# Performance work log

Hardware: AMD Instinct MI355X
Metric: run time of the kernel (lower is better)

Reference implementation:

```python
import jax, jax.numpy as jnp
import numpy as np

N_NODES = 10000
N_EDGES = 160000
IN_DIM = 256
HID = 128
HEADS = 8
OUT_DIM = 64
LN_EPS = 1e-5
NEG_SLOPE = 0.2


def _gat_layer(x, W, att_src, att_dst, bias, src, dst, heads, out_ch, n):
    # x: [N, F_in]; W: [F_in, heads*out_ch]; att_*: [heads, out_ch]; bias: [heads*out_ch]
    xl = (x @ W).reshape(n, heads, out_ch)              # [N, H, C]
    a_src = jnp.einsum('nhc,hc->nh', xl, att_src)        # [N, H]
    a_dst = jnp.einsum('nhc,hc->nh', xl, att_dst)        # [N, H]
    e = a_src[src] + a_dst[dst]                          # [E, H]
    e = jnp.where(e > 0, e, NEG_SLOPE * e)               # leaky_relu(0.2)
    e_max = jax.ops.segment_max(e, dst, num_segments=n)  # segment softmax (stable)
    e = jnp.exp(e - e_max[dst])
    denom = jax.ops.segment_sum(e, dst, num_segments=n)
    alpha = e / (denom[dst] + 1e-16)                     # [E, H]
    msg = xl[src] * alpha[:, :, None]                    # [E, H, C]
    out = jax.ops.segment_sum(msg, dst, num_segments=n)  # [N, H, C]
    return out.reshape(n, heads * out_ch) + bias


def setup_inputs() -> dict:
    key = jax.random.key(0)
    ks = jax.random.split(key, 12)
    s = 0.05
    inp = {
        'x': jax.random.normal(ks[0], (N_NODES, IN_DIM), dtype=jnp.float32),
        'edge_index': jax.random.randint(ks[1], (2, N_EDGES), 0, N_NODES, dtype=jnp.int32),
        'W1': jax.random.normal(ks[2], (IN_DIM, HEADS * HID), dtype=jnp.float32) * s,
        'att_src1': jax.random.normal(ks[3], (HEADS, HID), dtype=jnp.float32) * s,
        'att_dst1': jax.random.normal(ks[4], (HEADS, HID), dtype=jnp.float32) * s,
        'b1': jnp.zeros((HEADS * HID,), dtype=jnp.float32),
        'W2': jax.random.normal(ks[5], (HEADS * HID, OUT_DIM), dtype=jnp.float32) * s,
        'att_src2': jax.random.normal(ks[6], (1, OUT_DIM), dtype=jnp.float32) * s,
        'att_dst2': jax.random.normal(ks[7], (1, OUT_DIM), dtype=jnp.float32) * s,
        'b2': jnp.zeros((OUT_DIM,), dtype=jnp.float32),
        'gamma': jnp.ones((OUT_DIM,), dtype=jnp.float32),
        'beta': jnp.zeros((OUT_DIM,), dtype=jnp.float32),
    }
    return inp


def reference(x, edge_index, W1, att_src1, att_dst1, b1, W2, att_src2, att_dst2, b2, gamma, beta):
    n = x.shape[0]
    # GATConv adds self-loops by default
    loops = jnp.arange(n, dtype=edge_index.dtype)
    src = jnp.concatenate([edge_index[0], loops])
    dst = jnp.concatenate([edge_index[1], loops])
    h = _gat_layer(x, W1, att_src1, att_dst1, b1, src, dst, HEADS, HID, n)
    h = jax.nn.elu(h)  # dropout is identity in eval mode
    h = _gat_layer(h, W2, att_src2, att_dst2, b2, src, dst, 1, OUT_DIM, n)
    mu = jnp.mean(h, axis=-1, keepdims=True)
    var = jnp.mean(jnp.square(h - mu), axis=-1, keepdims=True)
    return (h - mu) / jnp.sqrt(var + LN_EPS) * gamma + beta
```

## Files before the change

### kernel.cpp

```cpp
#include <hip/hip_runtime.h>

#define N_NODES 10000
#define N_EDGES 160000
#define E_TOT   (N_EDGES + N_NODES)
#define IN_DIM  256
#define HID     128
#define HEADS   8
#define F1      (HEADS*HID)
#define OUT_DIM 64
#define LN_EPS  1e-5f
#define NEG_SLOPE 0.2f

typedef __attribute__((ext_vector_type(8))) short short8;
typedef __attribute__((ext_vector_type(4))) float f32x4;

static __device__ __forceinline__ float lrelu(float e){ return e > 0.f ? e : NEG_SLOPE*e; }

static __device__ __forceinline__ ushort f2bf(float f){
  union { float f; uint32_t u; } v; v.f = f;
  uint32_t u = v.u;
  return (ushort)((u + 0x7FFFu + ((u >> 16) & 1u)) >> 16);
}
static __device__ __forceinline__ float bf2f(ushort h){
  union { uint32_t u; float f; } v; v.u = ((uint32_t)h) << 16; return v.f;
}
#define BLO(u) bf2f((ushort)((u) & 0xffffu))
#define BHI(u) bf2f((ushort)((u) >> 16))


__global__ void k_cvt_x(const float* __restrict__ in, ushort* __restrict__ out, int n4){
  int i = blockIdx.x*blockDim.x + threadIdx.x;
  if (i >= n4) return;
  float4 v = *(const float4*)&in[(size_t)i*4];
  uint2 o;
  o.x = (uint32_t)f2bf(v.x) | ((uint32_t)f2bf(v.y) << 16);
  o.y = (uint32_t)f2bf(v.z) | ((uint32_t)f2bf(v.w) << 16);
  *(uint2*)&out[(size_t)i*4] = o;
}


__global__ __launch_bounds__(256) void k_tr(const float* __restrict__ W1, ushort* __restrict__ W1T,
                                            const float* __restrict__ W2, ushort* __restrict__ W2T){
  __shared__ float tile[64][65];
  int bid = blockIdx.x;
  const float* W; ushort* WT; int R, C, rt, ct;
  if (bid < 64){ W = W1; WT = W1T; R = IN_DIM; C = F1; rt = bid & 3; ct = bid >> 2; }
  else         { W = W2; WT = W2T; R = F1; C = OUT_DIM; rt = bid - 64; ct = 0; }
  int r0 = rt*64, c0 = ct*64;
  int t = threadIdx.x;
  int sub = t >> 4, q4 = (t & 15)*4;
  #pragma unroll
  for (int p = 0; p < 4; p++){
    int r = sub + p*16;
    float4 v = *(const float4*)&W[(size_t)(r0 + r)*C + c0 + q4];
    tile[r][q4]   = v.x; tile[r][q4+1] = v.y;
    tile[r][q4+2] = v.z; tile[r][q4+3] = v.w;
  }
  __syncthreads();
  #pragma unroll
  for (int p = 0; p < 4; p++){
    int c = sub + p*16;
    ushort h0 = f2bf(tile[q4+0][c]);
    ushort h1 = f2bf(tile[q4+1][c]);
    ushort h2 = f2bf(tile[q4+2][c]);
    ushort h3 = f2bf(tile[q4+3][c]);
    uint2 o;
    o.x = (uint32_t)h0 | ((uint32_t)h1 << 16);
    o.y = (uint32_t)h2 | ((uint32_t)h3 << 16);
    *(uint2*)&WT[(size_t)(c0 + c)*R + r0 + q4] = o;
  }
}


__global__ void k_hist(const int* __restrict__ ei, int* __restrict__ counts){
  int e = blockIdx.x*blockDim.x + threadIdx.x;
  if (e >= E_TOT) return;
  int dst = (e < N_EDGES) ? ei[N_EDGES + e] : (e - N_EDGES);
  atomicAdd(&counts[dst], 1);
}

__global__ __launch_bounds__(1024) void k_scan(const int* __restrict__ counts,
                                               int* __restrict__ offsets,
                                               int* __restrict__ cursor){
  __shared__ int part[1024];
  int tid = threadIdx.x;
  const int CH = (N_NODES + 1023)/1024;
  int base = tid*CH;
  int s = 0;
  #pragma unroll
  for (int i = 0; i < CH; i++){ int idx = base+i; if (idx < N_NODES) s += counts[idx]; }
  part[tid] = s;
  __syncthreads();
  for (int off = 1; off < 1024; off <<= 1){
    int v = (tid >= off) ? part[tid-off] : 0;
    __syncthreads();
    part[tid] += v;
    __syncthreads();
  }
  int run = part[tid] - s;
  for (int i = 0; i < CH; i++){
    int idx = base+i;
    if (idx < N_NODES){ offsets[idx] = run; cursor[idx] = run; run += counts[idx]; }
  }
}

__global__ void k_scatter(const int* __restrict__ ei, int* __restrict__ cursor,
                          int* __restrict__ csr_src){
  int e = blockIdx.x*blockDim.x + threadIdx.x;
  if (e >= E_TOT) return;
  int src, dst;
  if (e < N_EDGES){ src = ei[e]; dst = ei[N_EDGES + e]; }
  else            { src = e - N_EDGES; dst = src; }
  int pos = atomicAdd(&cursor[dst], 1);
  csr_src[pos] = src;
}


__global__ __launch_bounds__(256) void k_wav(const float* __restrict__ W1,
                                             const float* __restrict__ att_s,
                                             const float* __restrict__ att_d,
                                             float* __restrict__ w_as,
                                             float* __restrict__ w_ad){
  int wg = blockIdx.x*4 + (threadIdx.x >> 6);
  int lane = threadIdx.x & 63;
  int h = wg >> 8, i = wg & 255;
  if (h >= HEADS) return;
  int c = lane*2;
  float2 wv = *(const float2*)&W1[(size_t)i*F1 + h*HID + c];
  float2 as = *(const float2*)&att_s[h*HID + c];
  float2 ad = *(const float2*)&att_d[h*HID + c];
  float s = wv.x*as.x + wv.y*as.y;
  float d = wv.x*ad.x + wv.y*ad.y;
  #pragma unroll
  for (int o = 32; o > 0; o >>= 1){ s += __shfl_xor(s, o); d += __shfl_xor(d, o); }
  if (lane == 0){ w_as[h*IN_DIM + i] = s; w_ad[h*IN_DIM + i] = d; }
}


__global__ __launch_bounds__(256) void k_attv(const ushort* __restrict__ xb,
                                              const float* __restrict__ w_as,
                                              const float* __restrict__ w_ad,
                                              float* __restrict__ as1,
                                              float* __restrict__ ad1){
  int n = blockIdx.x*4 + (threadIdx.x >> 6);
  int lane = threadIdx.x & 63;
  if (n >= N_NODES) return;
  int c0 = lane*4;
  uint2 px = *(const uint2*)&xb[(size_t)n*IN_DIM + c0];
  float x0 = BLO(px.x), x1 = BHI(px.x), x2 = BLO(px.y), x3 = BHI(px.y);
  float s[HEADS], d[HEADS];
  #pragma unroll
  for (int h = 0; h < HEADS; h++){
    float4 ws = *(const float4*)&w_as[h*IN_DIM + c0];
    float4 wd = *(const float4*)&w_ad[h*IN_DIM + c0];
    s[h] = x0*ws.x + x1*ws.y + x2*ws.z + x3*ws.w;
    d[h] = x0*wd.x + x1*wd.y + x2*wd.z + x3*wd.w;
  }
  #pragma unroll
  for (int o = 32; o > 0; o >>= 1){
    #pragma unroll
    for (int h = 0; h < HEADS; h++){ s[h] += __shfl_xor(s[h], o); d[h] += __shfl_xor(d[h], o); }
  }
  if (lane == 0){
    #pragma unroll
    for (int h = 0; h < HEADS; h++){ as1[n*HEADS + h] = s[h]; ad1[n*HEADS + h] = d[h]; }
  }
}


__global__ __launch_bounds__(256) void k_prep1(const float* __restrict__ a_src,
                       const float* __restrict__ a_dst,
                       const int* __restrict__ offsets, const int* __restrict__ counts,
                       const int* __restrict__ csr, float* __restrict__ alpha){
  int n = blockIdx.x*4 + (threadIdx.x >> 6);
  int lane = threadIdx.x & 63;
  if (n >= N_NODES) return;
  int off = offsets[n], k = counts[n];
  float ad[HEADS];
  #pragma unroll
  for (int h = 0; h < HEADS; h++) ad[h] = a_dst[n*HEADS + h];

  float lm[HEADS];
  #pragma unroll
  for (int h = 0; h < HEADS; h++) lm[h] = -1e30f;
  for (int i = lane; i < k; i += 64){
    int s = csr[off + i];
    float4 v0 = *(const float4*)&a_src[s*HEADS];
    float4 v1 = *(const float4*)&a_src[s*HEADS + 4];
    lm[0] = fmaxf(lm[0], lrelu(v0.x + ad[0]));
    lm[1] = fmaxf(lm[1], lrelu(v0.y + ad[1]));
    lm[2] = fmaxf(lm[2], lrelu(v0.z + ad[2]));
    lm[3] = fmaxf(lm[3], lrelu(v0.w + ad[3]));
    lm[4] = fmaxf(lm[4], lrelu(v1.x + ad[4]));
    lm[5] = fmaxf(lm[5], lrelu(v1.y + ad[5]));
    lm[6] = fmaxf(lm[6], lrelu(v1.z + ad[6]));
    lm[7] = fmaxf(lm[7], lrelu(v1.w + ad[7]));
  }
  #pragma unroll
  for (int o = 32; o > 0; o >>= 1){
    #pragma unroll
    for (int h = 0; h < HEADS; h++) lm[h] = fmaxf(lm[h], __shfl_xor(lm[h], o));
  }

  float ls[HEADS];
  #pragma unroll
  for (int h = 0; h < HEADS; h++) ls[h] = 0.f;
  for (int i = lane; i < k; i += 64){
    int s = csr[off + i];
    float4 v0 = *(const float4*)&a_src[s*HEADS];
    float4 v1 = *(const float4*)&a_src[s*HEADS + 4];
    ls[0] += __expf(lrelu(v0.x + ad[0]) - lm[0]);
    ls[1] += __expf(lrelu(v0.y + ad[1]) - lm[1]);
    ls[2] += __expf(lrelu(v0.z + ad[2]) - lm[2]);
    ls[3] += __expf(lrelu(v0.w + ad[3]) - lm[3]);
    ls[4] += __expf(lrelu(v1.x + ad[4]) - lm[4]);
    ls[5] += __expf(lrelu(v1.y + ad[5]) - lm[5]);
    ls[6] += __expf(lrelu(v1.z + ad[6]) - lm[6]);
    ls[7] += __expf(lrelu(v1.w + ad[7]) - lm[7]);
  }
  #pragma unroll
  for (int o = 32; o > 0; o >>= 1){
    #pragma unroll
    for (int h = 0; h < HEADS; h++) ls[h] += __shfl_xor(ls[h], o);
  }
  float dinv[HEADS];
  #pragma unroll
  for (int h = 0; h < HEADS; h++) dinv[h] = 1.f/(ls[h] + 1e-16f);

  for (int i = lane; i < k; i += 64){
    int s = csr[off + i];
    float4 v0 = *(const float4*)&a_src[s*HEADS];
    float4 v1 = *(const float4*)&a_src[s*HEADS + 4];
    float4 w0, w1;
    w0.x = __expf(lrelu(v0.x + ad[0]) - lm[0])*dinv[0];
    w0.y = __expf(lrelu(v0.y + ad[1]) - lm[1])*dinv[1];
    w0.z = __expf(lrelu(v0.z + ad[2]) - lm[2])*dinv[2];
    w0.w = __expf(lrelu(v0.w + ad[3]) - lm[3])*dinv[3];
    w1.x = __expf(lrelu(v1.x + ad[4]) - lm[4])*dinv[4];
    w1.y = __expf(lrelu(v1.y + ad[5]) - lm[5])*dinv[5];
    w1.z = __expf(lrelu(v1.z + ad[6]) - lm[6])*dinv[6];
    w1.w = __expf(lrelu(v1.w + ad[7]) - lm[7])*dinv[7];
    *(float4*)&alpha[(size_t)(off + i)*HEADS]     = w0;
    *(float4*)&alpha[(size_t)(off + i)*HEADS + 4] = w1;
  }
}

__global__ __launch_bounds__(256) void k_prep2(const float* __restrict__ a_src,
                       const float* __restrict__ a_dst,
                       const int* __restrict__ offsets, const int* __restrict__ counts,
                       const int* __restrict__ csr, float* __restrict__ alpha){
  int n = blockIdx.x*4 + (threadIdx.x >> 6);
  int lane = threadIdx.x & 63;
  if (n >= N_NODES) return;
  int off = offsets[n], k = counts[n];
  float ad = a_dst[n];

  float lm = -1e30f;
  for (int i = lane; i < k; i += 64)
    lm = fmaxf(lm, lrelu(a_src[csr[off + i]] + ad));
  #pragma unroll
  for (int o = 32; o > 0; o >>= 1) lm = fmaxf(lm, __shfl_xor(lm, o));

  float ls = 0.f;
  for (int i = lane; i < k; i += 64)
    ls += __expf(lrelu(a_src[csr[off + i]] + ad) - lm);
  #pragma unroll
  for (int o = 32; o > 0; o >>= 1) ls += __shfl_xor(ls, o);
  float dinv = 1.f/(ls + 1e-16f);

  for (int i = lane; i < k; i += 64)
    alpha[off + i] = __expf(lrelu(a_src[csr[off + i]] + ad) - lm)*dinv;
}


__global__ __launch_bounds__(256) void k_aggpre(const ushort* __restrict__ xb,
                       const float* __restrict__ alpha,
                       const int* __restrict__ offsets, const int* __restrict__ counts,
                       const int* __restrict__ csr,
                       ushort* __restrict__ h1pre){
  int n = blockIdx.x;
  int off = offsets[n], k = counts[n];
  int t = threadIdx.x;
  int hc = t >> 5;
  int c0 = (t & 31)*8;
  float a[8];
  #pragma unroll
  for (int j = 0; j < 8; j++) a[j] = 0.f;

  int i = 0;
  for (; i + 1 < k; i += 2){
    int s0 = csr[off + i], s1 = csr[off + i + 1];
    float w0 = alpha[(size_t)(off + i)*HEADS + hc];
    float w1 = alpha[(size_t)(off + i + 1)*HEADS + hc];
    uint4 p0 = *(const uint4*)&xb[(size_t)s0*IN_DIM + c0];
    uint4 p1 = *(const uint4*)&xb[(size_t)s1*IN_DIM + c0];
    a[0] += w0*BLO(p0.x) + w1*BLO(p1.x);
    a[1] += w0*BHI(p0.x) + w1*BHI(p1.x);
    a[2] += w0*BLO(p0.y) + w1*BLO(p1.y);
    a[3] += w0*BHI(p0.y) + w1*BHI(p1.y);
    a[4] += w0*BLO(p0.z) + w1*BLO(p1.z);
    a[5] += w0*BHI(p0.z) + w1*BHI(p1.z);
    a[6] += w0*BLO(p0.w) + w1*BLO(p1.w);
    a[7] += w0*BHI(p0.w) + w1*BHI(p1.w);
  }
  if (i < k){
    int s0 = csr[off + i];
    float w0 = alpha[(size_t)(off + i)*HEADS + hc];
    uint4 p0 = *(const uint4*)&xb[(size_t)s0*IN_DIM + c0];
    a[0] += w0*BLO(p0.x);
    a[1] += w0*BHI(p0.x);
    a[2] += w0*BLO(p0.y);
    a[3] += w0*BHI(p0.y);
    a[4] += w0*BLO(p0.z);
    a[5] += w0*BHI(p0.z);
    a[6] += w0*BLO(p0.w);
    a[7] += w0*BHI(p0.w);
  }
  uint4 o;
  o.x = (uint32_t)f2bf(a[0]) | ((uint32_t)f2bf(a[1]) << 16);
  o.y = (uint32_t)f2bf(a[2]) | ((uint32_t)f2bf(a[3]) << 16);
  o.z = (uint32_t)f2bf(a[4]) | ((uint32_t)f2bf(a[5]) << 16);
  o.w = (uint32_t)f2bf(a[6]) | ((uint32_t)f2bf(a[7]) << 16);
  *(uint4*)&h1pre[(size_t)n*(HEADS*IN_DIM) + hc*IN_DIM + c0] = o;
}


template<int BM, int BN, int WAVES_N, int WM, int WN, int OUT_MODE, bool FUSE_ATT, int AHS>
__global__ __launch_bounds__(256) void k_gemm_bf16(const ushort* __restrict__ A,
                                                   const ushort* __restrict__ Bt,
                                                   void* __restrict__ Cout,
                                                   const float* __restrict__ bias,
                                                   const float* __restrict__ att_s,
                                                   const float* __restrict__ att_d,
                                                   float* __restrict__ out_as,
                                                   float* __restrict__ out_ad,
                                                   int M, int N, int K, int lda){
  const int LDK = 40;
  __shared__ ushort As[BM][LDK];
  __shared__ ushort Bs[BN][LDK];
  int tid = threadIdx.x;
  int lane = tid & 63, wid = tid >> 6;
  int wm = wid / WAVES_N, wn = wid % WAVES_N;
  int row0 = blockIdx.x * BM, col0 = blockIdx.y * BN;
  int aoff = blockIdx.y * AHS;
  int wrow = wm * (WM*16), wcol = wn * (WN*16);

  f32x4 acc[WM][WN];
  #pragma unroll
  for (int i = 0; i < WM; i++)
    #pragma unroll
    for (int j = 0; j < WN; j++)
      acc[i][j] = (f32x4){0.f, 0.f, 0.f, 0.f};

  int koff = (lane >> 4) * 8;
  int frow = lane & 15;
  int g = tid & 3, r = tid >> 2;

  for (int k0 = 0; k0 < K; k0 += 32){
    #pragma unroll
    for (int it = 0; it < BM/64; it++){
      int rr = r + it*64;
      int grow = row0 + rr;
      short8 v = (short8){0,0,0,0,0,0,0,0};
      if (grow < M) v = *(const short8*)&A[(size_t)grow*lda + aoff + k0 + g*8];
      *(short8*)&As[rr][g*8] = v;
    }
    #pragma unroll
    for (int it = 0; it < BN/64; it++){
      int rr = r + it*64;
      short8 v = *(const short8*)&Bt[(size_t)(col0 + rr)*K + k0 + g*8];
      *(short8*)&Bs[rr][g*8] = v;
    }
    __syncthreads();
    short8 af[WM], bf[WN];
    #pragma unroll
    for (int i = 0; i < WM; i++) af[i] = *(short8*)&As[wrow + i*16 + frow][koff];
    #pragma unroll
    for (int j = 0; j < WN; j++) bf[j] = *(short8*)&Bs[wcol + j*16 + frow][koff];
    #pragma unroll
    for (int i = 0; i < WM; i++)
      #pragma unroll
      for (int j = 0; j < WN; j++)
        acc[i][j] = __builtin_amdgcn_mfma_f32_16x16x32_bf16(af[i], bf[j], acc[i][j], 0, 0, 0);
    __syncthreads();
  }

  int lr = (lane >> 4) * 4, lc = lane & 15;

  #pragma unroll
  for (int i = 0; i < WM; i++){
    #pragma unroll
    for (int j = 0; j < WN; j++){
      int gc = col0 + wcol + j*16 + lc;
      #pragma unroll
      for (int q = 0; q < 4; q++){
        int gr = row0 + wrow + i*16 + lr + q;
        if (gr < M){
          if (OUT_MODE == 0){
            ((float*)Cout)[(size_t)gr*N + gc] = acc[i][j][q];
          } else if (OUT_MODE == 1){
            ((ushort*)Cout)[(size_t)gr*N + gc] = f2bf(acc[i][j][q]);
          } else {
            float v = acc[i][j][q] + bias[gc];
            v = v > 0.f ? v : __expf(v) - 1.f;
            ((ushort*)Cout)[(size_t)gr*N + gc] = f2bf(v);
          }
        }
      }
    }
  }

  if (FUSE_ATT){
    __shared__ float red_s[BM], red_d[BM];
    int head = blockIdx.y;
    int NH = gridDim.y;
    float asw[WN], adw[WN];
    #pragma unroll
    for (int j = 0; j < WN; j++){
      int c = wcol + j*16 + lc;
      asw[j] = att_s[head*BN + c];
      adw[j] = att_d[head*BN + c];
    }
    float ps[WM][4], pd[WM][4];
    #pragma unroll
    for (int i = 0; i < WM; i++){
      #pragma unroll
      for (int q = 0; q < 4; q++){
        float s = 0.f, d = 0.f;
        #pragma unroll
        for (int j = 0; j < WN; j++){ s += acc[i][j][q]*asw[j]; d += acc[i][j][q]*adw[j]; }
        #pragma unroll
        for (int o = 8; o > 0; o >>= 1){ s += __shfl_xor(s, o); d += __shfl_xor(d, o); }
        ps[i][q] = s; pd[i][q] = d;
      }
    }
    if (WAVES_N == 2){
      if (wn == 1 && lc == 0){
        #pragma unroll
        for (int i = 0; i < WM; i++)
          #pragma unroll
          for (int q = 0; q < 4; q++){
            red_s[wrow + i*16 + lr + q] = ps[i][q];
            red_d[wrow + i*16 + lr + q] = pd[i][q];
          }
      }
      __syncthreads();
      if (wn == 0 && lc == 0){
        #pragma unroll
        for (int i = 0; i < WM; i++)
          #pragma unroll
          for (int q = 0; q < 4; q++){
            ps[i][q] += red_s[wrow + i*16 + lr + q];
            pd[i][q] += red_d[wrow + i*16 + lr + q];
          }
      }
    }
    if (lc == 0 && (WAVES_N == 1 || wn == 0)){
      #pragma unroll
      for (int i = 0; i < WM; i++)
        #pragma unroll
        for (int q = 0; q < 4; q++){
          int gr = row0 + wrow + i*16 + lr + q;
          if (gr < M){
            out_as[(size_t)gr*NH + head] = ps[i][q];
            out_ad[(size_t)gr*NH + head] = pd[i][q];
          }
        }
    }
  }
}


__global__ __launch_bounds__(256) void k_agg2(const float* __restrict__ xl,
                       const float* __restrict__ alpha,
                       const int* __restrict__ offsets, const int* __restrict__ counts,
                       const int* __restrict__ csr, const float* __restrict__ b2,
                       const float* __restrict__ gamma, const float* __restrict__ beta,
                       float* __restrict__ out){
  int n = blockIdx.x*4 + (threadIdx.x >> 6);
  int lane = threadIdx.x & 63;
  if (n >= N_NODES) return;
  int off = offsets[n], k = counts[n];

  float acc0 = 0.f, acc1 = 0.f;
  int i = 0;
  for (; i + 3 < k; i += 4){
    int s0 = csr[off + i],     s1 = csr[off + i + 1];
    int s2 = csr[off + i + 2], s3 = csr[off + i + 3];
    float w0 = alpha[off + i],     w1 = alpha[off + i + 1];
    float w2 = alpha[off + i + 2], w3 = alpha[off + i + 3];
    acc0 += w0*xl[(size_t)s0*OUT_DIM + lane] + w1*xl[(size_t)s1*OUT_DIM + lane];
    acc1 += w2*xl[(size_t)s2*OUT_DIM + lane] + w3*xl[(size_t)s3*OUT_DIM + lane];
  }
  for (; i < k; i++)
    acc0 += alpha[off + i]*xl[(size_t)csr[off + i]*OUT_DIM + lane];
  float v = acc0 + acc1 + b2[lane];

  float mu = v;
  #pragma unroll
  for (int o = 32; o > 0; o >>= 1) mu += __shfl_xor(mu, o);
  mu *= (1.f/OUT_DIM);
  float d = v - mu;
  float var = d*d;
  #pragma unroll
  for (int o = 32; o > 0; o >>= 1) var += __shfl_xor(var, o);
  var *= (1.f/OUT_DIM);
  out[(size_t)n*OUT_DIM + lane] = d*rsqrtf(var + LN_EPS)*gamma[lane] + beta[lane];
}


extern "C" void kernel_launch(void* const* d_in, const int* in_sizes, int n_in,
                              void* d_out, int out_size, void* d_ws, size_t ws_size,
                              hipStream_t stream){
  const float* x        = (const float*)d_in[0];
  const int*   ei       = (const int*)  d_in[1];
  const float* W1       = (const float*)d_in[2];
  const float* att_src1 = (const float*)d_in[3];
  const float* att_dst1 = (const float*)d_in[4];
  const float* b1       = (const float*)d_in[5];
  const float* W2       = (const float*)d_in[6];
  const float* att_src2 = (const float*)d_in[7];
  const float* att_dst2 = (const float*)d_in[8];
  const float* b2       = (const float*)d_in[9];
  const float* gamma    = (const float*)d_in[10];
  const float* beta     = (const float*)d_in[11];
  float* out = (float*)d_out;

  char* w = (char*)d_ws;
  auto carve = [&](size_t bytes)->void*{
    void* p = (void*)w; w += (bytes + 255) & ~(size_t)255; return p;
  };
  ushort* xb      = (ushort*)carve((size_t)N_NODES*IN_DIM*sizeof(ushort));
  ushort* W1T     = (ushort*)carve((size_t)F1*IN_DIM*sizeof(ushort));
  ushort* W2T     = (ushort*)carve((size_t)OUT_DIM*F1*sizeof(ushort));
  ushort* h1pre   = (ushort*)carve((size_t)N_NODES*HEADS*IN_DIM*sizeof(ushort));
  ushort* h1b     = (ushort*)carve((size_t)N_NODES*F1*sizeof(ushort));
  float*  xl2     = (float*) carve((size_t)N_NODES*OUT_DIM*sizeof(float));
  float*  w_as    = (float*) carve((size_t)HEADS*IN_DIM*sizeof(float));
  float*  w_ad    = (float*) carve((size_t)HEADS*IN_DIM*sizeof(float));
  float*  as1     = (float*) carve((size_t)N_NODES*HEADS*sizeof(float));
  float*  ad1     = (float*) carve((size_t)N_NODES*HEADS*sizeof(float));
  float*  as2     = (float*) carve((size_t)N_NODES*sizeof(float));
  float*  ad2     = (float*) carve((size_t)N_NODES*sizeof(float));
  float*  alpha1  = (float*) carve((size_t)E_TOT*HEADS*sizeof(float));
  float*  alpha2  = (float*) carve((size_t)E_TOT*sizeof(float));
  int*    counts  = (int*)   carve((size_t)N_NODES*sizeof(int));
  int*    offsets = (int*)   carve((size_t)N_NODES*sizeof(int));
  int*    cursor  = (int*)   carve((size_t)N_NODES*sizeof(int));
  int*    csr     = (int*)   carve((size_t)E_TOT*sizeof(int));

  k_cvt_x<<<(N_NODES*IN_DIM/4 + 255)/256, 256, 0, stream>>>(x, xb, N_NODES*IN_DIM/4);
  k_tr<<<80, 256, 0, stream>>>(W1, W1T, W2, W2T);
  hipMemsetAsync(counts, 0, (size_t)N_NODES*sizeof(int), stream);

  k_hist   <<<(E_TOT+255)/256, 256, 0, stream>>>(ei, counts);
  k_scan   <<<1, 1024, 0, stream>>>(counts, offsets, cursor);
  k_scatter<<<(E_TOT+255)/256, 256, 0, stream>>>(ei, cursor, csr);

  const int NB4 = (N_NODES + 3)/4;
  const int MT128 = (N_NODES + 127)/128;
  const int MT64  = (N_NODES + 63)/64;

  k_wav <<<512, 256, 0, stream>>>(W1, att_src1, att_dst1, w_as, w_ad);
  k_attv<<<NB4, 256, 0, stream>>>(xb, w_as, w_ad, as1, ad1);
  k_prep1<<<NB4, 256, 0, stream>>>(as1, ad1, offsets, counts, csr, alpha1);
  k_aggpre<<<N_NODES, 256, 0, stream>>>(xb, alpha1, offsets, counts, csr, h1pre);
  k_gemm_bf16<128, 128, 2, 4, 4, 2, false, IN_DIM><<<dim3(MT128, HEADS), 256, 0, stream>>>(
      h1pre, W1T, h1b, b1, nullptr, nullptr, nullptr, nullptr,
      N_NODES, F1, IN_DIM, HEADS*IN_DIM);

  k_gemm_bf16<64, 64, 2, 2, 2, 0, true, 0><<<dim3(MT64, 1), 256, 0, stream>>>(
      h1b, W2T, xl2, nullptr, att_src2, att_dst2, as2, ad2,
      N_NODES, OUT_DIM, F1, F1);
  k_prep2<<<NB4, 256, 0, stream>>>(as2, ad2, offsets, counts, csr, alpha2);
  k_agg2<<<NB4, 256, 0, stream>>>(xl2, alpha2, offsets, counts, csr, b2, gamma, beta, out);
}
```

Measured before the change: 241.0 us.

## Fuse prologue kernels, fold layer-2 softmax into aggregation, stage aggpre rows in LDS

Merges the x conversion, the weight transposes and the attention-weight projection into one prologue launch. Removes k_prep2 by computing the layer-2 segment softmax inside k_agg2, keeping edge sources and weights in registers and broadcasting them with shuffles. k_aggpre now loads 8 neighbour rows cooperatively into shared memory, so each row of x is fetched once for all heads rather than once per head group. This cuts kernel launches and global traffic, at the cost of extra block syncs and register pressure.

```diff
diff --git a/kernel.cpp b/kernel.cpp
--- a/kernel.cpp
+++ b/kernel.cpp
@@ -28,47 +28,63 @@
 #define BHI(u) bf2f((ushort)((u) >> 16))
 
 
-__global__ void k_cvt_x(const float* __restrict__ in, ushort* __restrict__ out, int n4){
-  int i = blockIdx.x*blockDim.x + threadIdx.x;
-  if (i >= n4) return;
-  float4 v = *(const float4*)&in[(size_t)i*4];
-  uint2 o;
-  o.x = (uint32_t)f2bf(v.x) | ((uint32_t)f2bf(v.y) << 16);
-  o.y = (uint32_t)f2bf(v.z) | ((uint32_t)f2bf(v.w) << 16);
-  *(uint2*)&out[(size_t)i*4] = o;
-}
-
-
-__global__ __launch_bounds__(256) void k_tr(const float* __restrict__ W1, ushort* __restrict__ W1T,
-                                            const float* __restrict__ W2, ushort* __restrict__ W2T){
+__global__ __launch_bounds__(256) void k_prologue(const float* __restrict__ x, ushort* __restrict__ xb,
+                          const float* __restrict__ W1, ushort* __restrict__ W1T,
+                          const float* __restrict__ W2, ushort* __restrict__ W2T,
+                          const float* __restrict__ att_s1, const float* __restrict__ att_d1,
+                          float* __restrict__ w_as, float* __restrict__ w_ad){
   __shared__ float tile[64][65];
+  const int NB_CVT = (N_NODES*IN_DIM/4)/256;
   int bid = blockIdx.x;
-  const float* W; ushort* WT; int R, C, rt, ct;
-  if (bid < 64){ W = W1; WT = W1T; R = IN_DIM; C = F1; rt = bid & 3; ct = bid >> 2; }
-  else         { W = W2; WT = W2T; R = F1; C = OUT_DIM; rt = bid - 64; ct = 0; }
-  int r0 = rt*64, c0 = ct*64;
-  int t = threadIdx.x;
-  int sub = t >> 4, q4 = (t & 15)*4;
-  #pragma unroll
-  for (int p = 0; p < 4; p++){
-    int r = sub + p*16;
-    float4 v = *(const float4*)&W[(size_t)(r0 + r)*C + c0 + q4];
-    tile[r][q4]   = v.x; tile[r][q4+1] = v.y;
-    tile[r][q4+2] = v.z; tile[r][q4+3] = v.w;
-  }
-  __syncthreads();
-  #pragma unroll
-  for (int p = 0; p < 4; p++){
-    int c = sub + p*16;
-    ushort h0 = f2bf(tile[q4+0][c]);
-    ushort h1 = f2bf(tile[q4+1][c]);
-    ushort h2 = f2bf(tile[q4+2][c]);
-    ushort h3 = f2bf(tile[q4+3][c]);
+  if (bid < NB_CVT){
+    int i = bid*256 + threadIdx.x;
+    float4 v = *(const float4*)&x[(size_t)i*4];
     uint2 o;
-    o.x = (uint32_t)h0 | ((uint32_t)h1 << 16);
-    o.y = (uint32_t)h2 | ((uint32_t)h3 << 16);
-    *(uint2*)&WT[(size_t)(c0 + c)*R + r0 + q4] = o;
-  }
+    o.x = (uint32_t)f2bf(v.x) | ((uint32_t)f2bf(v.y) << 16);
+    o.y = (uint32_t)f2bf(v.z) | ((uint32_t)f2bf(v.w) << 16);
+    *(uint2*)&xb[(size_t)i*4] = o;
+    return;
+  }
+  bid -= NB_CVT;
+  if (bid < 80){
+    const float* W; ushort* WT; int R, C, rt, ct;
+    if (bid < 64){ W = W1; WT = W1T; R = IN_DIM; C = F1; rt = bid & 3; ct = bid >> 2; }
+    else         { W = W2; WT = W2T; R = F1; C = OUT_DIM; rt = bid - 64; ct = 0; }
+    int r0 = rt*64, c0 = ct*64;
+    int t = threadIdx.x;
+    int sub = t >> 4, q4 = (t & 15)*4;
+    #pragma unroll
+    for (int p = 0; p < 4; p++){
+      int r = sub + p*16;
+      float4 v = *(const float4*)&W[(size_t)(r0 + r)*C + c0 + q4];
+      tile[r][q4]   = v.x; tile[r][q4+1] = v.y;
+      tile[r][q4+2] = v.z; tile[r][q4+3] = v.w;
+    }
+    __syncthreads();
+    #pragma unroll
+    for (int p = 0; p < 4; p++){
+      int c = sub + p*16;
+      uint2 o;
+      o.x = (uint32_t)f2bf(tile[q4+0][c]) | ((uint32_t)f2bf(tile[q4+1][c]) << 16);
+      o.y = (uint32_t)f2bf(tile[q4+2][c]) | ((uint32_t)f2bf(tile[q4+3][c]) << 16);
+      *(uint2*)&WT[(size_t)(c0 + c)*R + r0 + q4] = o;
+    }
+    return;
+  }
+  bid -= 80;
+  int wg = bid*4 + (threadIdx.x >> 6);
+  int lane = threadIdx.x & 63;
+  int h = wg >> 8, i = wg & 255;
+  if (h >= HEADS) return;
+  int c = lane*2;
+  float2 wv = *(const float2*)&W1[(size_t)i*F1 + h*HID + c];
+  float2 as = *(const float2*)&att_s1[h*HID + c];
+  float2 ad = *(const float2*)&att_d1[h*HID + c];
+  float s = wv.x*as.x + wv.y*as.y;
+  float d = wv.x*ad.x + wv.y*ad.y;
+  #pragma unroll
+  for (int o = 32; o > 0; o >>= 1){ s += __shfl_xor(s, o); d += __shfl_xor(d, o); }
+  if (lane == 0){ w_as[h*IN_DIM + i] = s; w_ad[h*IN_DIM + i] = d; }
 }
 
 
@@ -113,27 +129,6 @@
   else            { src = e - N_EDGES; dst = src; }
   int pos = atomicAdd(&cursor[dst], 1);
   csr_src[pos] = src;
-}
-
-
-__global__ __launch_bounds__(256) void k_wav(const float* __restrict__ W1,
-                                             const float* __restrict__ att_s,
-                                             const float* __restrict__ att_d,
-                                             float* __restrict__ w_as,
-                                             float* __restrict__ w_ad){
-  int wg = blockIdx.x*4 + (threadIdx.x >> 6);
-  int lane = threadIdx.x & 63;
-  int h = wg >> 8, i = wg & 255;
-  if (h >= HEADS) return;
-  int c = lane*2;
-  float2 wv = *(const float2*)&W1[(size_t)i*F1 + h*HID + c];
-  float2 as = *(const float2*)&att_s[h*HID + c];
-  float2 ad = *(const float2*)&att_d[h*HID + c];
-  float s = wv.x*as.x + wv.y*as.y;
-  float d = wv.x*ad.x + wv.y*ad.y;
-  #pragma unroll
-  for (int o = 32; o > 0; o >>= 1){ s += __shfl_xor(s, o); d += __shfl_xor(d, o); }
-  if (lane == 0){ w_as[h*IN_DIM + i] = s; w_ad[h*IN_DIM + i] = d; }
 }
 
 
@@ -245,83 +240,48 @@
   }
 }
 
-__global__ __launch_bounds__(256) void k_prep2(const float* __restrict__ a_src,
-                       const float* __restrict__ a_dst,
-                       const int* __restrict__ offsets, const int* __restrict__ counts,
-                       const int* __restrict__ csr, float* __restrict__ alpha){
-  int n = blockIdx.x*4 + (threadIdx.x >> 6);
-  int lane = threadIdx.x & 63;
-  if (n >= N_NODES) return;
-  int off = offsets[n], k = counts[n];
-  float ad = a_dst[n];
-
-  float lm = -1e30f;
-  for (int i = lane; i < k; i += 64)
-    lm = fmaxf(lm, lrelu(a_src[csr[off + i]] + ad));
-  #pragma unroll
-  for (int o = 32; o > 0; o >>= 1) lm = fmaxf(lm, __shfl_xor(lm, o));
-
-  float ls = 0.f;
-  for (int i = lane; i < k; i += 64)
-    ls += __expf(lrelu(a_src[csr[off + i]] + ad) - lm);
-  #pragma unroll
-  for (int o = 32; o > 0; o >>= 1) ls += __shfl_xor(ls, o);
-  float dinv = 1.f/(ls + 1e-16f);
-
-  for (int i = lane; i < k; i += 64)
-    alpha[off + i] = __expf(lrelu(a_src[csr[off + i]] + ad) - lm)*dinv;
-}
-
 
 __global__ __launch_bounds__(256) void k_aggpre(const ushort* __restrict__ xb,
                        const float* __restrict__ alpha,
                        const int* __restrict__ offsets, const int* __restrict__ counts,
                        const int* __restrict__ csr,
                        ushort* __restrict__ h1pre){
+  __shared__ ushort xs[8][IN_DIM + 8];
+  __shared__ float  als[8][HEADS];
   int n = blockIdx.x;
   int off = offsets[n], k = counts[n];
   int t = threadIdx.x;
-  int hc = t >> 5;
-  int c0 = (t & 31)*8;
+  int g = t >> 5;
+  int c = t & 31;
   float a[8];
   #pragma unroll
   for (int j = 0; j < 8; j++) a[j] = 0.f;
 
-  int i = 0;
-  for (; i + 1 < k; i += 2){
-    int s0 = csr[off + i], s1 = csr[off + i + 1];
-    float w0 = alpha[(size_t)(off + i)*HEADS + hc];
-    float w1 = alpha[(size_t)(off + i + 1)*HEADS + hc];
-    uint4 p0 = *(const uint4*)&xb[(size_t)s0*IN_DIM + c0];
-    uint4 p1 = *(const uint4*)&xb[(size_t)s1*IN_DIM + c0];
-    a[0] += w0*BLO(p0.x) + w1*BLO(p1.x);
-    a[1] += w0*BHI(p0.x) + w1*BHI(p1.x);
-    a[2] += w0*BLO(p0.y) + w1*BLO(p1.y);
-    a[3] += w0*BHI(p0.y) + w1*BHI(p1.y);
-    a[4] += w0*BLO(p0.z) + w1*BLO(p1.z);
-    a[5] += w0*BHI(p0.z) + w1*BHI(p1.z);
-    a[6] += w0*BLO(p0.w) + w1*BLO(p1.w);
-    a[7] += w0*BHI(p0.w) + w1*BHI(p1.w);
-  }
-  if (i < k){
-    int s0 = csr[off + i];
-    float w0 = alpha[(size_t)(off + i)*HEADS + hc];
-    uint4 p0 = *(const uint4*)&xb[(size_t)s0*IN_DIM + c0];
-    a[0] += w0*BLO(p0.x);
-    a[1] += w0*BHI(p0.x);
-    a[2] += w0*BLO(p0.y);
-    a[3] += w0*BHI(p0.y);
-    a[4] += w0*BLO(p0.z);
-    a[5] += w0*BHI(p0.z);
-    a[6] += w0*BLO(p0.w);
-    a[7] += w0*BHI(p0.w);
+  for (int i0 = 0; i0 < k; i0 += 8){
+    int ne = k - i0; if (ne > 8) ne = 8;
+    if (g < ne){
+      int s = csr[off + i0 + g];
+      *(uint4*)&xs[g][c*8] = *(const uint4*)&xb[(size_t)s*IN_DIM + c*8];
+    }
+    if (t < 64 && (t >> 3) < ne)
+      als[t >> 3][t & 7] = alpha[(size_t)(off + i0 + (t >> 3))*HEADS + (t & 7)];
+    __syncthreads();
+    for (int e = 0; e < ne; e++){
+      float w = als[e][g];
+      uint4 p = *(const uint4*)&xs[e][c*8];
+      a[0] += w*BLO(p.x); a[1] += w*BHI(p.x);
+      a[2] += w*BLO(p.y); a[3] += w*BHI(p.y);
+      a[4] += w*BLO(p.z); a[5] += w*BHI(p.z);
+      a[6] += w*BLO(p.w); a[7] += w*BHI(p.w);
+    }
+    __syncthreads();
   }
   uint4 o;
   o.x = (uint32_t)f2bf(a[0]) | ((uint32_t)f2bf(a[1]) << 16);
   o.y = (uint32_t)f2bf(a[2]) | ((uint32_t)f2bf(a[3]) << 16);
   o.z = (uint32_t)f2bf(a[4]) | ((uint32_t)f2bf(a[5]) << 16);
   o.w = (uint32_t)f2bf(a[6]) | ((uint32_t)f2bf(a[7]) << 16);
-  *(uint4*)&h1pre[(size_t)n*(HEADS*IN_DIM) + hc*IN_DIM + c0] = o;
+  *(uint4*)&h1pre[(size_t)n*(HEADS*IN_DIM) + g*IN_DIM + c*8] = o;
 }
 
 
@@ -417,9 +377,9 @@
     float asw[WN], adw[WN];
     #pragma unroll
     for (int j = 0; j < WN; j++){
-      int c = wcol + j*16 + lc;
-      asw[j] = att_s[head*BN + c];
-      adw[j] = att_d[head*BN + c];
+      int c2 = wcol + j*16 + lc;
+      asw[j] = att_s[head*BN + c2];
+      adw[j] = att_d[head*BN + c2];
     }
     float ps[WM][4], pd[WM][4];
     #pragma unroll
@@ -472,28 +432,72 @@
 
 
 __global__ __launch_bounds__(256) void k_agg2(const float* __restrict__ xl,
-                       const float* __restrict__ alpha,
+                       const float* __restrict__ a_src, const float* __restrict__ a_dst,
                        const int* __restrict__ offsets, const int* __restrict__ counts,
                        const int* __restrict__ csr, const float* __restrict__ b2,
                        const float* __restrict__ gamma, const float* __restrict__ beta,
                        float* __restrict__ out){
+  const int L = 4;
   int n = blockIdx.x*4 + (threadIdx.x >> 6);
   int lane = threadIdx.x & 63;
   if (n >= N_NODES) return;
   int off = offsets[n], k = counts[n];
-
+  float ad = a_dst[n];
+
+  int   sv[L];
+  float ev[L];
+  float lm = -1e30f;
+  #pragma unroll
+  for (int j = 0; j < L; j++){
+    int i = lane + 64*j;
+    sv[j] = 0; ev[j] = -1e30f;
+    if (i < k){
+      sv[j] = csr[off + i];
+      ev[j] = lrelu(a_src[sv[j]] + ad);
+      lm = fmaxf(lm, ev[j]);
+    }
+  }
+  for (int i = lane + 64*L; i < k; i += 64)
+    lm = fmaxf(lm, lrelu(a_src[csr[off + i]] + ad));
+  #pragma unroll
+  for (int o = 32; o > 0; o >>= 1) lm = fmaxf(lm, __shfl_xor(lm, o));
+
+  float wv[L];
+  float ls = 0.f;
+  #pragma unroll
+  for (int j = 0; j < L; j++){
+    wv[j] = 0.f;
+    if (lane + 64*j < k){ wv[j] = __expf(ev[j] - lm); ls += wv[j]; }
+  }
+  for (int i = lane + 64*L; i < k; i += 64)
+    ls += __expf(lrelu(a_src[csr[off + i]] + ad) - lm);
+  #pragma unroll
+  for (int o = 32; o > 0; o >>= 1) ls += __shfl_xor(ls, o);
+  float dinv = 1.f/(ls + 1e-16f);
+  #pragma unroll
+  for (int j = 0; j < L; j++) wv[j] *= dinv;
+
+  int kc = k < 64*L ? k : 64*L;
   float acc0 = 0.f, acc1 = 0.f;
   int i = 0;
-  for (; i + 3 < k; i += 4){
-    int s0 = csr[off + i],     s1 = csr[off + i + 1];
-    int s2 = csr[off + i + 2], s3 = csr[off + i + 3];
-    float w0 = alpha[off + i],     w1 = alpha[off + i + 1];
-    float w2 = alpha[off + i + 2], w3 = alpha[off + i + 3];
-    acc0 += w0*xl[(size_t)s0*OUT_DIM + lane] + w1*xl[(size_t)s1*OUT_DIM + lane];
-    acc1 += w2*xl[(size_t)s2*OUT_DIM + lane] + w3*xl[(size_t)s3*OUT_DIM + lane];
-  }
-  for (; i < k; i++)
-    acc0 += alpha[off + i]*xl[(size_t)csr[off + i]*OUT_DIM + lane];
+  for (; i + 1 < kc; i += 2){
+    int   s0 = __shfl(sv[i>>6], i & 63);
+    float w0 = __shfl(wv[i>>6], i & 63);
+    int   s1 = __shfl(sv[(i+1)>>6], (i+1) & 63);
+    float w1 = __shfl(wv[(i+1)>>6], (i+1) & 63);
+    acc0 += w0*xl[(size_t)s0*OUT_DIM + lane];
+    acc1 += w1*xl[(size_t)s1*OUT_DIM + lane];
+  }
+  for (; i < kc; i++){
+    int   s0 = __shfl(sv[i>>6], i & 63);
+    float w0 = __shfl(wv[i>>6], i & 63);
+    acc0 += w0*xl[(size_t)s0*OUT_DIM + lane];
+  }
+  for (; i < k; i++){
+    int s0 = csr[off + i];
+    float w0 = __expf(lrelu(a_src[s0] + ad) - lm)*dinv;
+    acc0 += w0*xl[(size_t)s0*OUT_DIM + lane];
+  }
   float v = acc0 + acc1 + b2[lane];
 
   float mu = v;
@@ -543,14 +547,14 @@
   float*  as2     = (float*) carve((size_t)N_NODES*sizeof(float));
   float*  ad2     = (float*) carve((size_t)N_NODES*sizeof(float));
   float*  alpha1  = (float*) carve((size_t)E_TOT*HEADS*sizeof(float));
-  float*  alpha2  = (float*) carve((size_t)E_TOT*sizeof(float));
   int*    counts  = (int*)   carve((size_t)N_NODES*sizeof(int));
   int*    offsets = (int*)   carve((size_t)N_NODES*sizeof(int));
   int*    cursor  = (int*)   carve((size_t)N_NODES*sizeof(int));
   int*    csr     = (int*)   carve((size_t)E_TOT*sizeof(int));
 
-  k_cvt_x<<<(N_NODES*IN_DIM/4 + 255)/256, 256, 0, stream>>>(x, xb, N_NODES*IN_DIM/4);
-  k_tr<<<80, 256, 0, stream>>>(W1, W1T, W2, W2T);
+  const int NB_PRO = (N_NODES*IN_DIM/4)/256 + 80 + 512;
+  k_prologue<<<NB_PRO, 256, 0, stream>>>(x, xb, W1, W1T, W2, W2T,
+                                         att_src1, att_dst1, w_as, w_ad);
   hipMemsetAsync(counts, 0, (size_t)N_NODES*sizeof(int), stream);
 
   k_hist   <<<(E_TOT+255)/256, 256, 0, stream>>>(ei, counts);
@@ -561,7 +565,6 @@
   const int MT128 = (N_NODES + 127)/128;
   const int MT64  = (N_NODES + 63)/64;
 
-  k_wav <<<512, 256, 0, stream>>>(W1, att_src1, att_dst1, w_as, w_ad);
   k_attv<<<NB4, 256, 0, stream>>>(xb, w_as, w_ad, as1, ad1);
   k_prep1<<<NB4, 256, 0, stream>>>(as1, ad1, offsets, counts, csr, alpha1);
   k_aggpre<<<N_NODES, 256, 0, stream>>>(xb, alpha1, offsets, counts, csr, h1pre);
@@ -572,6 +575,5 @@
   k_gemm_bf16<64, 64, 2, 2, 2, 0, true, 0><<<dim3(MT64, 1), 256, 0, stream>>>(
       h1b, W2T, xl2, nullptr, att_src2, att_dst2, as2, ad2,
       N_NODES, OUT_DIM, F1, F1);
-  k_prep2<<<NB4, 256, 0, stream>>>(as2, ad2, offsets, counts, csr, alpha2);
-  k_agg2<<<NB4, 256, 0, stream>>>(xl2, alpha2, offsets, counts, csr, b2, gamma, beta, out);
-}
+  k_agg2<<<NB4, 256, 0, stream>>>(xl2, as2, ad2, offsets, counts, csr, b2, gamma, beta, out);
+}
```

New measurement: 233.5 us. 1.03x faster.
